# Kernel tuning notes

Measured on AMD Instinct MI355X. Metric: run time of the kernel, lower is better.

The kernel has to match this reference:

```python
import jax, jax.numpy as jnp
import numpy as np

EPS = 0.0  # torch code divides by norms directly (no eps); inputs are randn so norms > 0


def setup_inputs() -> dict:
    key = jax.random.key(0)
    ks = jax.random.split(key, 16)
    B, C, H, W = 16, 64, 128, 128
    DIM = 4 * C  # 256
    f32 = jnp.float32
    inp = {
        "low": jax.random.normal(ks[0], (B, C, H, W), f32),
        "high": jax.random.normal(ks[1], (B, C, H, W), f32),
        "flow": jax.random.normal(ks[2], (B, C, H, W), f32),
        "feedback": jax.random.normal(ks[3], (B, C, H, W), f32),
        # GCN(4, 64, 64): single graph-conv layer, relu(adj @ x @ W + b)
        "Wgcn": jax.random.normal(ks[4], (C, C), f32) * 0.05,
        "bgcn": jnp.zeros((C,), f32),
        # four SE fc heads: Linear(DIM -> C) + sigmoid
        "W1": jax.random.normal(ks[5], (C, DIM), f32) * 0.05,
        "b1": jnp.zeros((C,), f32),
        "W2": jax.random.normal(ks[6], (C, DIM), f32) * 0.05,
        "b2": jnp.zeros((C,), f32),
        "W3": jax.random.normal(ks[7], (C, DIM), f32) * 0.05,
        "b3": jnp.zeros((C,), f32),
        "W4": jax.random.normal(ks[8], (C, DIM), f32) * 0.05,
        "b4": jnp.zeros((C,), f32),
        # gate: 1x1 Conv2d(DIM -> 64) stored as dense [64, DIM]
        "Wgate": jax.random.normal(ks[9], (C, DIM), f32) * 0.05,
        "bgate": jnp.zeros((C,), f32),
    }
    return inp


def reference(low, high, flow, feedback, Wgcn, bgcn, W1, b1, W2, b2, W3, b3, W4, b4, Wgate, bgate):
    B, C, H, W = low.shape
    # adaptive avg pool(1) of concat([low,high,flow,feedback], dim=1) then view(B,4,C)
    combined_fc = jnp.stack([
        low.mean(axis=(2, 3)),
        high.mean(axis=(2, 3)),
        flow.mean(axis=(2, 3)),
        feedback.mean(axis=(2, 3)),
    ], axis=1)  # [B, 4, C]
    # cosine-similarity adjacency  [B, 4, 4]
    norm = jnp.linalg.norm(combined_fc, axis=2, keepdims=True)  # [B,4,1]
    mul = jnp.einsum('bic,bjc->bij', combined_fc, combined_fc)
    batch_adj = mul / (norm * norm.transpose(0, 2, 1))
    # tiny GCN: relu(adj @ x @ W + b)  -> feat_cat = flatten over nodes
    h = jax.nn.relu(jnp.einsum('bij,bjc,cd->bid', batch_adj, combined_fc, Wgcn) + bgcn)  # [B,4,C]
    feat_cat = h.reshape(B, 4 * C)  # [B, 256]
    sig = jax.nn.sigmoid
    e1 = sig(feat_cat @ W1.T + b1)[:, :, None, None]  # [B,C,1,1]
    e2 = sig(feat_cat @ W2.T + b2)[:, :, None, None]
    e3 = sig(feat_cat @ W3.T + b3)[:, :, None, None]
    e4 = sig(feat_cat @ W4.T + b4)[:, :, None, None]
    wa = low + e2 * high + e3 * flow + e4 * feedback
    wb = e1 * low + high + e3 * flow + e4 * feedback
    wc = e1 * low + e2 * high + flow + e4 * feedback
    wd = e1 * low + e2 * high + e3 * flow + feedback
    feat = jnp.concatenate([wa, wb, wc, wd], axis=1)  # [B, 4C, H, W]
    # 1x1 conv == channel GEMM
    out = jnp.einsum('bchw,oc->bohw', feat, Wgate) + bgate[None, :, None, None]
    return out
```

## Files before the change

### kernel.cpp

```cpp
#include <hip/hip_runtime.h>
#include <cmath>

#define BB 16
#define CC 64
#define PP 16384

typedef float f32x4 __attribute__((ext_vector_type(4)));
typedef float f32x2 __attribute__((ext_vector_type(2)));

__global__ __launch_bounds__(256) void k_means(const float* __restrict__ low,
                                               const float* __restrict__ high,
                                               const float* __restrict__ flow,
                                               const float* __restrict__ fb,
                                               float* __restrict__ cf) {
    int blk = blockIdx.x;
    int b = blk >> 8, t = (blk >> 6) & 3, c = blk & 63;
    const float* in = (t == 0) ? low : (t == 1) ? high : (t == 2) ? flow : fb;
    const float4* p = (const float4*)(in + ((size_t)(b * CC + c)) * PP);
    int tid = threadIdx.x;

    float s = 0.f;
    #pragma unroll
    for (int i = 0; i < 16; ++i) {
        float4 v = p[tid + i * 256];
        s += (v.x + v.y) + (v.z + v.w);
    }
    #pragma unroll
    for (int off = 32; off > 0; off >>= 1) s += __shfl_down(s, off, 64);

    __shared__ float r[4];
    if ((tid & 63) == 0) r[tid >> 6] = s;
    __syncthreads();
    if (tid == 0)
        cf[(b * 4 + t) * CC + c] = ((r[0] + r[1]) + (r[2] + r[3])) * (1.0f / PP);
}

__global__ __launch_bounds__(256) void k_small(const float* __restrict__ cf,
    const float* __restrict__ Wgcn, const float* __restrict__ bgcn,
    const float* __restrict__ W1, const float* __restrict__ b1,
    const float* __restrict__ W2, const float* __restrict__ b2,
    const float* __restrict__ W3, const float* __restrict__ b3,
    const float* __restrict__ W4, const float* __restrict__ b4,
    const float* __restrict__ Wgate,
    float* __restrict__ Amat) {
    int b = blockIdx.x;
    int tid = threadIdx.x;
    int lane = tid & 63;
    int wid = tid >> 6;
    __shared__ float x[4][64];
    __shared__ float nrm[4];
    __shared__ float adj[16];
    __shared__ float y[4][64];
    __shared__ float fc[256];
    __shared__ float e[4][64];

    x[wid][lane] = cf[b * 256 + tid];
    __syncthreads();

    if (tid < 4) {
        float s = 0.f;
        for (int c = 0; c < 64; ++c) s += x[tid][c] * x[tid][c];
        nrm[tid] = sqrtf(s);
    }
    __syncthreads();

    if (tid < 16) {
        int i = tid >> 2, j = tid & 3;
        float s = 0.f;
        for (int c = 0; c < 64; ++c) s += x[i][c] * x[j][c];
        adj[tid] = s / (nrm[i] * nrm[j]);
    }
    __syncthreads();

    {
        float s = 0.f;
        #pragma unroll
        for (int j = 0; j < 4; ++j) s += adj[wid * 4 + j] * x[j][lane];
        y[wid][lane] = s;
    }
    __syncthreads();

    {
        float s = bgcn[lane];
        for (int c = 0; c < 64; ++c) s += y[wid][c] * Wgcn[c * 64 + lane];
        fc[wid * 64 + lane] = fmaxf(s, 0.f);
    }
    __syncthreads();

    {
        const float* Wk = (wid == 0) ? W1 : (wid == 1) ? W2 : (wid == 2) ? W3 : W4;
        const float* bk = (wid == 0) ? b1 : (wid == 1) ? b2 : (wid == 2) ? b3 : b4;
        float4 fv = *(const float4*)&fc[lane * 4];
        for (int c = 0; c < 64; ++c) {
            float4 w = *(const float4*)(Wk + c * 256 + lane * 4);
            float part = (w.x * fv.x + w.y * fv.y) + (w.z * fv.z + w.w * fv.w);
            #pragma unroll
            for (int off = 32; off > 0; off >>= 1)
                part += __shfl_down(part, off, 64);
            if (lane == 0) {
                float s = part + bk[c];
                e[wid][c] = 1.f / (1.f + expf(-s));
            }
        }
    }
    __syncthreads();

    {
        int t = wid, o = lane;
        const float* wrow = Wgate + o * 256;
        float* Ab = Amat + b * 16384 + t * 4096;
        #pragma unroll 4
        for (int c4 = 0; c4 < 64; c4 += 4) {
            float4 w0 = *(const float4*)(wrow + c4);
            float4 w1 = *(const float4*)(wrow + 64 + c4);
            float4 w2 = *(const float4*)(wrow + 128 + c4);
            float4 w3 = *(const float4*)(wrow + 192 + c4);
            float4 wt = (t == 0) ? w0 : (t == 1) ? w1 : (t == 2) ? w2 : w3;
            float4 sm = make_float4((w0.x + w1.x) + (w2.x + w3.x),
                                    (w0.y + w1.y) + (w2.y + w3.y),
                                    (w0.z + w1.z) + (w2.z + w3.z),
                                    (w0.w + w1.w) + (w2.w + w3.w));
            Ab[(c4 + 0) * 64 + o] = wt.x + e[t][c4 + 0] * (sm.x - wt.x);
            Ab[(c4 + 1) * 64 + o] = wt.y + e[t][c4 + 1] * (sm.y - wt.y);
            Ab[(c4 + 2) * 64 + o] = wt.z + e[t][c4 + 2] * (sm.z - wt.z);
            Ab[(c4 + 3) * 64 + o] = wt.w + e[t][c4 + 3] * (sm.w - wt.w);
        }
    }
}

__global__ __launch_bounds__(256, 3) void k_gemm(const float* __restrict__ low,
    const float* __restrict__ high, const float* __restrict__ flow,
    const float* __restrict__ fb, const float* __restrict__ Amat,
    const float* __restrict__ bgate, float* __restrict__ out) {
    int blk = blockIdx.x;
    int b = blk >> 6;
    int tile = blk & 63;
    int tid = threadIdx.x;
    int pt = tid & 63;
    int og = __builtin_amdgcn_readfirstlane(tid >> 6);
    int p0 = tile * 256 + pt * 4;

    size_t xoff = (size_t)b * (CC * PP) + p0;
    const float* px[4] = {low + xoff, high + xoff, flow + xoff, fb + xoff};
    const float* Ab = Amat + b * 16384 + og * 16;

    f32x2 acc[8][4];
    #pragma unroll
    for (int j2 = 0; j2 < 8; ++j2)
        #pragma unroll
        for (int q = 0; q < 4; ++q) acc[j2][q] = (f32x2)(0.f);

    #pragma unroll 2
    for (int c = 0; c < 64; ++c) {
        f32x4 xv[4];
        #pragma unroll
        for (int t = 0; t < 4; ++t)
            xv[t] = *(const f32x4*)(px[t] + (size_t)c * PP);
        #pragma unroll
        for (int t = 0; t < 4; ++t) {
            const f32x2* ap = (const f32x2*)(Ab + t * 4096 + c * 64);
            #pragma unroll
            for (int q = 0; q < 4; ++q) {
                f32x2 xb;
                xb.x = xv[t][q]; xb.y = xv[t][q];
                #pragma unroll
                for (int j2 = 0; j2 < 8; ++j2)
                    acc[j2][q] = __builtin_elementwise_fma(ap[j2], xb, acc[j2][q]);
            }
        }
    }

    #pragma unroll
    for (int j2 = 0; j2 < 8; ++j2) {
        #pragma unroll
        for (int par = 0; par < 2; ++par) {
            int o = og * 16 + j2 * 2 + par;
            float bg = bgate[o];
            f32x4 r;
            r.x = acc[j2][0][par] + bg;
            r.y = acc[j2][1][par] + bg;
            r.z = acc[j2][2][par] + bg;
            r.w = acc[j2][3][par] + bg;
            *(f32x4*)(out + ((size_t)(b * CC + o)) * PP + p0) = r;
        }
    }
}

extern "C" void kernel_launch(void* const* d_in, const int* in_sizes, int n_in,
                              void* d_out, int out_size, void* d_ws, size_t ws_size,
                              hipStream_t stream) {
    const float* low  = (const float*)d_in[0];
    const float* high = (const float*)d_in[1];
    const float* flow = (const float*)d_in[2];
    const float* fb   = (const float*)d_in[3];
    const float* Wgcn = (const float*)d_in[4];
    const float* bgcn = (const float*)d_in[5];
    const float* W1   = (const float*)d_in[6];
    const float* b1   = (const float*)d_in[7];
    const float* W2   = (const float*)d_in[8];
    const float* b2   = (const float*)d_in[9];
    const float* W3   = (const float*)d_in[10];
    const float* b3   = (const float*)d_in[11];
    const float* W4   = (const float*)d_in[12];
    const float* b4   = (const float*)d_in[13];
    const float* Wgate = (const float*)d_in[14];
    const float* bgate = (const float*)d_in[15];
    float* out = (float*)d_out;

    float* cf   = (float*)d_ws;
    float* Amat = (float*)d_ws + 4096;

    k_means<<<BB * 4 * CC, 256, 0, stream>>>(low, high, flow, fb, cf);
    k_small<<<BB, 256, 0, stream>>>(cf, Wgcn, bgcn, W1, b1, W2, b2, W3, b3,
                                    W4, b4, Wgate, Amat);
    k_gemm<<<BB * CC, 256, 0, stream>>>(low, high, flow, fb, Amat, bgate, out);
}
```

Before: 429.7 us.

## Use split-bf16 MFMA (3-pass) for the channel GEMM instead of FP32 FMAs

Rewrites the per-batch 256->64 channel GEMM to run on matrix cores with bf16 16x16x32 MFMA. Each fp32 value is split into high and low bf16 halves, and three MFMA products (hi*hi, hi*lo, lo*hi) are accumulated to approximate fp32 accuracy. This aims to cut the VALU FMA cost. In exchange it adds split arithmetic, scalar strided global loads of 16 consecutive floats per row, non-vectorized stores, and a lower launch-bounds occupancy hint.

```diff
diff --git a/kernel.cpp b/kernel.cpp
--- a/kernel.cpp
+++ b/kernel.cpp
@@ -6,7 +6,9 @@
 #define PP 16384
 
 typedef float f32x4 __attribute__((ext_vector_type(4)));
-typedef float f32x2 __attribute__((ext_vector_type(2)));
+typedef short bf16x8 __attribute__((ext_vector_type(8)));
+typedef int i32x4 __attribute__((ext_vector_type(4)));
+typedef unsigned int u32;
 
 __global__ __launch_bounds__(256) void k_means(const float* __restrict__ low,
                                                const float* __restrict__ high,
@@ -128,7 +130,18 @@
     }
 }
 
-__global__ __launch_bounds__(256, 3) void k_gemm(const float* __restrict__ low,
+__device__ __forceinline__ void split_pair(float v0, float v1, u32& hi, u32& lo) {
+    u32 u0 = __builtin_bit_cast(u32, v0);
+    u32 u1 = __builtin_bit_cast(u32, v1);
+    u32 h0 = u0 & 0xFFFF0000u;
+    u32 h1 = u1 & 0xFFFF0000u;
+    hi = (h0 >> 16) | h1;
+    float l0 = v0 - __builtin_bit_cast(float, h0);
+    float l1 = v1 - __builtin_bit_cast(float, h1);
+    lo = (__builtin_bit_cast(u32, l0) >> 16) | (__builtin_bit_cast(u32, l1) & 0xFFFF0000u);
+}
+
+__global__ __launch_bounds__(256, 2) void k_gemm(const float* __restrict__ low,
     const float* __restrict__ high, const float* __restrict__ flow,
     const float* __restrict__ fb, const float* __restrict__ Amat,
     const float* __restrict__ bgate, float* __restrict__ out) {
@@ -136,54 +149,93 @@
     int b = blk >> 6;
     int tile = blk & 63;
     int tid = threadIdx.x;
-    int pt = tid & 63;
-    int og = __builtin_amdgcn_readfirstlane(tid >> 6);
-    int p0 = tile * 256 + pt * 4;
-
-    size_t xoff = (size_t)b * (CC * PP) + p0;
+    int lane = tid & 63;
+    int wv = tid >> 6;
+    int l15 = lane & 15;
+    int kq = (lane >> 4) << 3;
+
+    int pbase = tile * 256 + wv * 64 + l15;
+    size_t xoff = (size_t)b * (CC * PP) + (size_t)kq * PP + pbase;
     const float* px[4] = {low + xoff, high + xoff, flow + xoff, fb + xoff};
-    const float* Ab = Amat + b * 16384 + og * 16;
-
-    f32x2 acc[8][4];
-    #pragma unroll
-    for (int j2 = 0; j2 < 8; ++j2)
-        #pragma unroll
-        for (int q = 0; q < 4; ++q) acc[j2][q] = (f32x2)(0.f);
-
-    #pragma unroll 2
-    for (int c = 0; c < 64; ++c) {
-        f32x4 xv[4];
-        #pragma unroll
-        for (int t = 0; t < 4; ++t)
-            xv[t] = *(const f32x4*)(px[t] + (size_t)c * PP);
-        #pragma unroll
-        for (int t = 0; t < 4; ++t) {
-            const f32x2* ap = (const f32x2*)(Ab + t * 4096 + c * 64);
-            #pragma unroll
-            for (int q = 0; q < 4; ++q) {
-                f32x2 xb;
-                xb.x = xv[t][q]; xb.y = xv[t][q];
-                #pragma unroll
-                for (int j2 = 0; j2 < 8; ++j2)
-                    acc[j2][q] = __builtin_elementwise_fma(ap[j2], xb, acc[j2][q]);
+    const float* Ap = Amat + b * 16384 + kq * 64 + l15;
+
+    f32x4 acc[4][4];
+    #pragma unroll
+    for (int i = 0; i < 4; ++i)
+        #pragma unroll
+        for (int j = 0; j < 4; ++j) acc[i][j] = (f32x4)(0.f);
+
+    #pragma unroll
+    for (int t = 0; t < 4; ++t) {
+        const float* xp = px[t];
+        #pragma unroll
+        for (int h = 0; h < 2; ++h) {
+            float xr[4][8];
+            #pragma unroll
+            for (int pt = 0; pt < 4; ++pt)
+                #pragma unroll
+                for (int j = 0; j < 8; ++j)
+                    xr[pt][j] = xp[(size_t)(h * 32 + j) * PP + pt * 16];
+
+            float ar[4][8];
+            #pragma unroll
+            for (int ot = 0; ot < 4; ++ot)
+                #pragma unroll
+                for (int j = 0; j < 8; ++j)
+                    ar[ot][j] = Ap[(t * 64 + h * 32 + j) * 64 + ot * 16];
+
+            bf16x8 xh[4], xl[4], ah[4], al[4];
+            #pragma unroll
+            for (int pt = 0; pt < 4; ++pt) {
+                i32x4 hd, ld;
+                #pragma unroll
+                for (int d = 0; d < 4; ++d) {
+                    u32 hi, lo;
+                    split_pair(xr[pt][2 * d], xr[pt][2 * d + 1], hi, lo);
+                    hd[d] = (int)hi; ld[d] = (int)lo;
+                }
+                xh[pt] = __builtin_bit_cast(bf16x8, hd);
+                xl[pt] = __builtin_bit_cast(bf16x8, ld);
             }
-        }
-    }
-
-    #pragma unroll
-    for (int j2 = 0; j2 < 8; ++j2) {
-        #pragma unroll
-        for (int par = 0; par < 2; ++par) {
-            int o = og * 16 + j2 * 2 + par;
+            #pragma unroll
+            for (int ot = 0; ot < 4; ++ot) {
+                i32x4 hd, ld;
+                #pragma unroll
+                for (int d = 0; d < 4; ++d) {
+                    u32 hi, lo;
+                    split_pair(ar[ot][2 * d], ar[ot][2 * d + 1], hi, lo);
+                    hd[d] = (int)hi; ld[d] = (int)lo;
+                }
+                ah[ot] = __builtin_bit_cast(bf16x8, hd);
+                al[ot] = __builtin_bit_cast(bf16x8, ld);
+            }
+
+            #pragma unroll
+            for (int ot = 0; ot < 4; ++ot)
+                #pragma unroll
+                for (int pt = 0; pt < 4; ++pt) {
+                    acc[ot][pt] = __builtin_amdgcn_mfma_f32_16x16x32_bf16(
+                        ah[ot], xh[pt], acc[ot][pt], 0, 0, 0);
+                    acc[ot][pt] = __builtin_amdgcn_mfma_f32_16x16x32_bf16(
+                        ah[ot], xl[pt], acc[ot][pt], 0, 0, 0);
+                    acc[ot][pt] = __builtin_amdgcn_mfma_f32_16x16x32_bf16(
+                        al[ot], xh[pt], acc[ot][pt], 0, 0, 0);
+                }
+        }
+    }
+
+    int rg = lane >> 4;
+    size_t obase = (size_t)b * (CC * PP) + (size_t)pbase;
+    #pragma unroll
+    for (int ot = 0; ot < 4; ++ot)
+        #pragma unroll
+        for (int r = 0; r < 4; ++r) {
+            int o = ot * 16 + rg * 4 + r;
             float bg = bgate[o];
-            f32x4 r;
-            r.x = acc[j2][0][par] + bg;
-            r.y = acc[j2][1][par] + bg;
-            r.z = acc[j2][2][par] + bg;
-            r.w = acc[j2][3][par] + bg;
-            *(f32x4*)(out + ((size_t)(b * CC + o)) * PP + p0) = r;
-        }
-    }
+            #pragma unroll
+            for (int pt = 0; pt < 4; ++pt)
+                out[obase + (size_t)o * PP + pt * 16] = acc[ot][pt][r] + bg;
+        }
 }
 
 extern "C" void kernel_launch(void* const* d_in, const int* in_sizes, int n_in,
```

Result: faster. 391.9 us (-8.8%).
